# Optimization experiments

Measured on AMD Instinct MI355X. Metric: run time of the kernel, lower is better.

## Reference

```python
import jax, jax.numpy as jnp
import numpy as np

IN_F = 4096
OUT_F = 11008
GROUP = 128
NGROUPS = IN_F // GROUP
MAX_INT = 15  # 2**4 - 1


def setup_inputs() -> dict:
    key = jax.random.key(0)
    k1, k2, k3, k4, k5 = jax.random.split(key, 5)
    x = jax.random.normal(k1, (4, 2048, IN_F), dtype=jnp.float32)
    qweight = jax.random.randint(k2, (OUT_F, IN_F), 0, MAX_INT + 1, dtype=jnp.int32)
    scales = jax.random.uniform(k3, (OUT_F, NGROUPS), dtype=jnp.float32) * 0.01 + 1e-4
    zeros = jax.random.uniform(k4, (OUT_F, NGROUPS), dtype=jnp.float32) * MAX_INT
    b = jax.random.normal(k5, (OUT_F,), dtype=jnp.float32)
    return {"x": x, "qweight": qweight, "scales": scales, "zeros": zeros, "b": b}


def reference(x, qweight, scales, zeros, b):
    # Group-wise dequantization: W[o, i] = (q[o, i] - zeros[o, g(i)]) * scales[o, g(i)]
    s_rep = jnp.repeat(scales, GROUP, axis=1)  # [OUT_F, IN_F]
    z_rep = jnp.repeat(zeros, GROUP, axis=1)   # [OUT_F, IN_F]
    w_fp = (qweight.astype(x.dtype) - z_rep.astype(x.dtype)) * s_rep.astype(x.dtype)
    # F.linear: x @ W.T + b
    out = jnp.einsum('bsi,oi->bso', x, w_fp) + b.astype(x.dtype)
    return out
```

## Files before the change

kernel.cpp:

```cpp
#include <hip/hip_runtime.h>
#include <hip/hip_bf16.h>


#define K_DIM 4096
#define N_DIM 11008
#define M_DIM 8192
#define NGRP 32

typedef __bf16 bf16x8 __attribute__((ext_vector_type(8)));
typedef float f32x4 __attribute__((ext_vector_type(4)));
typedef unsigned short u16x8 __attribute__((ext_vector_type(8)));

__device__ __forceinline__ unsigned short f2bf(float f) {
  unsigned u = __builtin_bit_cast(unsigned, f);
  return (unsigned short)((u + 0x7FFFu + ((u >> 16) & 1u)) >> 16);
}

__device__ __forceinline__ void gload_lds16(const void* g, void* l) {
  __builtin_amdgcn_global_load_lds(
      (const __attribute__((address_space(1))) unsigned int*)(unsigned long long)g,
      (__attribute__((address_space(3))) unsigned int*)(unsigned int)(unsigned long long)l,
      16, 0, 0);
}

__global__ __launch_bounds__(256) void cvt_x_kernel(const float4* __restrict__ x4,
                                                    u16x8* __restrict__ xb) {
  int i = blockIdx.x * 256 + threadIdx.x;
  float4 a = x4[2 * i], b = x4[2 * i + 1];
  u16x8 r;
  r[0] = f2bf(a.x); r[1] = f2bf(a.y); r[2] = f2bf(a.z); r[3] = f2bf(a.w);
  r[4] = f2bf(b.x); r[5] = f2bf(b.y); r[6] = f2bf(b.z); r[7] = f2bf(b.w);
  xb[i] = r;
}

__global__ __launch_bounds__(256) void dequant_kernel(const int4* __restrict__ q4,
                                                      const float* __restrict__ scales,
                                                      const float* __restrict__ zeros,
                                                      u16x8* __restrict__ wb) {
  int t = blockIdx.x * 256 + threadIdx.x;
  int o = t >> 9;
  int j8 = t & 511;
  int g = j8 >> 4;
  float s = scales[o * NGRP + g];
  float z = zeros[o * NGRP + g];
  float nzs = -z * s;
  int4 qa = q4[2 * t], qb = q4[2 * t + 1];
  u16x8 r;
  r[0] = f2bf(fmaf((float)qa.x, s, nzs));
  r[1] = f2bf(fmaf((float)qa.y, s, nzs));
  r[2] = f2bf(fmaf((float)qa.z, s, nzs));
  r[3] = f2bf(fmaf((float)qa.w, s, nzs));
  r[4] = f2bf(fmaf((float)qb.x, s, nzs));
  r[5] = f2bf(fmaf((float)qb.y, s, nzs));
  r[6] = f2bf(fmaf((float)qb.z, s, nzs));
  r[7] = f2bf(fmaf((float)qb.w, s, nzs));
  wb[t] = r;
}


#define BAR() __builtin_amdgcn_s_barrier()
#define SCHED0() __builtin_amdgcn_sched_barrier(0)

__global__ __launch_bounds__(512, 2) void gemm_kernel(const unsigned short* __restrict__ A,
                                                      const unsigned short* __restrict__ B,
                                                      const float* __restrict__ bias,
                                                      float* __restrict__ C) {
  extern __shared__ unsigned short smem[];
  unsigned short* sAb = smem;
  unsigned short* sBb = smem + 32768;

  const int bid = blockIdx.x;
  const int swz = (bid & 7) * 172 + (bid >> 3);
  const int tm = swz / 43, tn = swz % 43;

  const int tid = threadIdx.x;
  const int w = tid >> 6, l = tid & 63;
  const int wr = w >> 2, wc = w & 3;

  const int dsto = w * 512 + l * 8;
  const int gs = (l & 7) ^ (l >> 3);
  const unsigned short* gA = A + (size_t)(tm * 256 + (tid >> 3)) * K_DIM + gs * 8;
  const unsigned short* gB = B + (size_t)(tn * 256 + (tid >> 3)) * K_DIM + gs * 8;

#define STG_A(tt, h, dst)                                                       \
  do {                                                                          \
    const unsigned short* _s = gA + (size_t)(h) * 128 * K_DIM + (tt) * 64;      \
    gload_lds16(_s, (dst) + dsto);                                              \
    gload_lds16(_s + 64 * K_DIM, (dst) + 4096 + dsto);                          \
  } while (0)
#define STG_B(tt, h, dst)                                                       \
  do {                                                                          \
    const unsigned short* _s = gB + (size_t)(h) * 128 * K_DIM + (tt) * 64;      \
    gload_lds16(_s, (dst) + dsto);                                              \
    gload_lds16(_s + 64 * K_DIM, (dst) + 4096 + dsto);                          \
  } while (0)

  const int fr = l & 15, sb = l >> 4, x7 = l & 7;
  const int abase = (wr * 64 + fr) * 64;
  const int bbase = (wc * 32 + fr) * 64;
  const int k0 = (sb ^ x7) * 8;
  const int k1 = ((sb + 4) ^ x7) * 8;

  bf16x8 av[4][2], bva[2][2], bvb[2][2];
  f32x4 acc[8][4] = {};

#define READ_A(half)                                                     \
  {                                                                      \
    _Pragma("unroll") for (int m = 0; m < 4; ++m) {                      \
      av[m][0] = *(const bf16x8*)((half) + abase + m * 1024 + k0);       \
      av[m][1] = *(const bf16x8*)((half) + abase + m * 1024 + k1);       \
    }                                                                    \
  }
#define READ_B(half, arr)                                                \
  {                                                                      \
    _Pragma("unroll") for (int n = 0; n < 2; ++n) {                      \
      arr[n][0] = *(const bf16x8*)((half) + bbase + n * 1024 + k0);      \
      arr[n][1] = *(const bf16x8*)((half) + bbase + n * 1024 + k1);      \
    }                                                                    \
  }
#define MFMA_Q(mh, nh, arr)                                                        \
  {                                                                                \
    __builtin_amdgcn_s_setprio(1);                                                 \
    _Pragma("unroll") for (int kk = 0; kk < 2; ++kk)                               \
    _Pragma("unroll") for (int m = 0; m < 4; ++m)                                  \
    _Pragma("unroll") for (int nn = 0; nn < 2; ++nn)                               \
      acc[(mh)*4 + m][(nh)*2 + nn] = __builtin_amdgcn_mfma_f32_16x16x32_bf16(      \
          av[m][kk], arr[nn][kk], acc[(mh)*4 + m][(nh)*2 + nn], 0, 0, 0);          \
    __builtin_amdgcn_s_setprio(0);                                                 \
  }

  STG_A(0, 0, sAb);
  STG_A(0, 1, sAb + 8192);
  STG_B(0, 0, sBb);
  STG_B(0, 1, sBb + 8192);
  STG_A(1, 0, sAb + 16384);
  STG_B(1, 1, sBb + 16384 + 8192);
  asm volatile("s_waitcnt vmcnt(4)" ::: "memory");
  BAR();
  SCHED0();

#pragma unroll 2
  for (int t = 0; t < 64; ++t) {
    const int p = t & 1;
    unsigned short* cA = sAb + p * 16384;
    unsigned short* cB = sBb + p * 16384;
    unsigned short* nA = sAb + (p ^ 1) * 16384;
    unsigned short* nB = sBb + (p ^ 1) * 16384;

    READ_A(cA);
    READ_B(cB, bva);
    if (t < 63) STG_A(t + 1, 1, nA + 8192);
    BAR();
    SCHED0();
    MFMA_Q(0, 0, bva);

    READ_B(cB + 8192, bvb);
    if (t < 63) STG_B(t + 1, 0, nB);
    BAR();
    SCHED0();
    MFMA_Q(0, 1, bvb);

    READ_A(cA + 8192);
    if (t < 62) STG_A(t + 2, 0, cA);
    BAR();
    SCHED0();
    MFMA_Q(1, 1, bvb);

    if (t < 62) STG_B(t + 2, 1, cB + 8192);
    MFMA_Q(1, 0, bva);
    if (t < 62) {
      asm volatile("s_waitcnt vmcnt(4)" ::: "memory");
    } else {
      asm volatile("s_waitcnt vmcnt(0)" ::: "memory");
    }
    BAR();
    SCHED0();
  }

  const int r0 = tm * 256 + wr * 64 + sb * 4;
  const int c0 = tn * 256 + wc * 32 + fr;
#pragma unroll
  for (int n = 0; n < 4; ++n) {
    const int col = c0 + (n >> 1) * 128 + (n & 1) * 16;
    const float bv = bias[col];
#pragma unroll
    for (int mi = 0; mi < 8; ++mi) {
      const int row = r0 + (mi >> 2) * 128 + (mi & 3) * 16;
#pragma unroll
      for (int jj = 0; jj < 4; ++jj)
        C[(size_t)(row + jj) * N_DIM + col] = acc[mi][n][jj] + bv;
    }
  }
}

extern "C" void kernel_launch(void* const* d_in, const int* in_sizes, int n_in,
                              void* d_out, int out_size, void* d_ws, size_t ws_size,
                              hipStream_t stream) {
  const float* x = (const float*)d_in[0];
  const int* qw = (const int*)d_in[1];
  const float* sc = (const float*)d_in[2];
  const float* zr = (const float*)d_in[3];
  const float* bs = (const float*)d_in[4];
  float* out = (float*)d_out;

  const size_t xb_bytes = (size_t)M_DIM * K_DIM * 2;
  const size_t wb_bytes = (size_t)N_DIM * K_DIM * 2;
  if (ws_size < xb_bytes + wb_bytes) return;

  unsigned short* xb = (unsigned short*)d_ws;
  unsigned short* wb = (unsigned short*)((char*)d_ws + xb_bytes);

  (void)hipFuncSetAttribute((const void*)gemm_kernel,
                            hipFuncAttributeMaxDynamicSharedMemorySize, 131072);

  cvt_x_kernel<<<(M_DIM * K_DIM / 8) / 256, 256, 0, stream>>>((const float4*)x, (u16x8*)xb);
  dequant_kernel<<<(N_DIM * K_DIM / 8) / 256, 256, 0, stream>>>((const int4*)qw, sc, zr,
                                                                (u16x8*)wb);
  gemm_kernel<<<(M_DIM / 256) * (N_DIM / 256), 512, 131072, stream>>>(xb, wb, bs, out);
}
```

Before: 733.9 us.

## Load B operand directly from global into registers, halve LDS usage

```diff
diff --git a/kernel.cpp b/kernel.cpp
--- a/kernel.cpp
+++ b/kernel.cpp
@@ -66,8 +66,8 @@
                                                       const float* __restrict__ bias,
                                                       float* __restrict__ C) {
   extern __shared__ unsigned short smem[];
-  unsigned short* sAb = smem;
-  unsigned short* sBb = smem + 32768;
+  unsigned short* s0 = smem;
+  unsigned short* s1 = smem + 16384;
 
   const int bid = blockIdx.x;
   const int swz = (bid & 7) * 172 + (bid >> 3);
@@ -80,7 +80,6 @@
   const int dsto = w * 512 + l * 8;
   const int gs = (l & 7) ^ (l >> 3);
   const unsigned short* gA = A + (size_t)(tm * 256 + (tid >> 3)) * K_DIM + gs * 8;
-  const unsigned short* gB = B + (size_t)(tn * 256 + (tid >> 3)) * K_DIM + gs * 8;
 
 #define STG_A(tt, h, dst)                                                       \
   do {                                                                          \
@@ -88,20 +87,16 @@
     gload_lds16(_s, (dst) + dsto);                                              \
     gload_lds16(_s + 64 * K_DIM, (dst) + 4096 + dsto);                          \
   } while (0)
-#define STG_B(tt, h, dst)                                                       \
-  do {                                                                          \
-    const unsigned short* _s = gB + (size_t)(h) * 128 * K_DIM + (tt) * 64;      \
-    gload_lds16(_s, (dst) + dsto);                                              \
-    gload_lds16(_s + 64 * K_DIM, (dst) + 4096 + dsto);                          \
-  } while (0)
 
   const int fr = l & 15, sb = l >> 4, x7 = l & 7;
   const int abase = (wr * 64 + fr) * 64;
-  const int bbase = (wc * 32 + fr) * 64;
   const int k0 = (sb ^ x7) * 8;
   const int k1 = ((sb + 4) ^ x7) * 8;
 
-  bf16x8 av[4][2], bva[2][2], bvb[2][2];
+  const unsigned short* gBbase = B + (size_t)(tn * 256 + wc * 32 + fr) * K_DIM + sb * 8;
+
+  bf16x8 av[4][2];
+  bf16x8 bE[2][2][2], bO[2][2][2];
   f32x4 acc[8][4] = {};
 
 #define READ_A(half)                                                     \
@@ -111,70 +106,73 @@
       av[m][1] = *(const bf16x8*)((half) + abase + m * 1024 + k1);       \
     }                                                                    \
   }
-#define READ_B(half, arr)                                                \
-  {                                                                      \
-    _Pragma("unroll") for (int n = 0; n < 2; ++n) {                      \
-      arr[n][0] = *(const bf16x8*)((half) + bbase + n * 1024 + k0);      \
-      arr[n][1] = *(const bf16x8*)((half) + bbase + n * 1024 + k1);      \
-    }                                                                    \
-  }
-#define MFMA_Q(mh, nh, arr)                                                        \
+#define LOAD_B(dst, kp)                                                            \
+  {                                                                                \
+    _Pragma("unroll") for (int h = 0; h < 2; ++h)                                  \
+    _Pragma("unroll") for (int nn = 0; nn < 2; ++nn)                               \
+    _Pragma("unroll") for (int kk = 0; kk < 2; ++kk)                               \
+      dst[h][nn][kk] = *(const bf16x8*)((kp) + (size_t)h * (128 * K_DIM) +         \
+                                        nn * (16 * K_DIM) + kk * 32);              \
+  }
+#define MFMA_Q(mh, h, B2)                                                          \
   {                                                                                \
     __builtin_amdgcn_s_setprio(1);                                                 \
     _Pragma("unroll") for (int kk = 0; kk < 2; ++kk)                               \
     _Pragma("unroll") for (int m = 0; m < 4; ++m)                                  \
     _Pragma("unroll") for (int nn = 0; nn < 2; ++nn)                               \
-      acc[(mh)*4 + m][(nh)*2 + nn] = __builtin_amdgcn_mfma_f32_16x16x32_bf16(      \
-          av[m][kk], arr[nn][kk], acc[(mh)*4 + m][(nh)*2 + nn], 0, 0, 0);          \
+      acc[(mh)*4 + m][(h)*2 + nn] = __builtin_amdgcn_mfma_f32_16x16x32_bf16(       \
+          av[m][kk], B2[nn][kk], acc[(mh)*4 + m][(h)*2 + nn], 0, 0, 0);            \
     __builtin_amdgcn_s_setprio(0);                                                 \
   }
 
-  STG_A(0, 0, sAb);
-  STG_A(0, 1, sAb + 8192);
-  STG_B(0, 0, sBb);
-  STG_B(0, 1, sBb + 8192);
-  STG_A(1, 0, sAb + 16384);
-  STG_B(1, 1, sBb + 16384 + 8192);
-  asm volatile("s_waitcnt vmcnt(4)" ::: "memory");
+  STG_A(0, 0, s0);
+  STG_A(0, 1, s0 + 8192);
+  SCHED0();
+  LOAD_B(bE, gBbase);
+  asm volatile("s_waitcnt vmcnt(8)" ::: "memory");
   BAR();
   SCHED0();
 
-#pragma unroll 2
-  for (int t = 0; t < 64; ++t) {
-    const int p = t & 1;
-    unsigned short* cA = sAb + p * 16384;
-    unsigned short* cB = sBb + p * 16384;
-    unsigned short* nA = sAb + (p ^ 1) * 16384;
-    unsigned short* nB = sBb + (p ^ 1) * 16384;
-
-    READ_A(cA);
-    READ_B(cB, bva);
-    if (t < 63) STG_A(t + 1, 1, nA + 8192);
+  const unsigned short* kp = gBbase;
+  for (int tt = 0; tt < 32; ++tt) {
+    const int t1 = 2 * tt + 1;
+
+    READ_A(s0);
+    STG_A(t1, 0, s1);
+    STG_A(t1, 1, s1 + 8192);
+    SCHED0();
+    MFMA_Q(0, 0, bE[0]);
+    MFMA_Q(0, 1, bE[1]);
+    SCHED0();
+    LOAD_B(bO, kp + 64);
+    SCHED0();
+    READ_A(s0 + 8192);
+    MFMA_Q(1, 1, bE[1]);
+    MFMA_Q(1, 0, bE[0]);
+    asm volatile("s_waitcnt vmcnt(8)" ::: "memory");
     BAR();
     SCHED0();
-    MFMA_Q(0, 0, bva);
-
-    READ_B(cB + 8192, bvb);
-    if (t < 63) STG_B(t + 1, 0, nB);
-    BAR();
-    SCHED0();
-    MFMA_Q(0, 1, bvb);
-
-    READ_A(cA + 8192);
-    if (t < 62) STG_A(t + 2, 0, cA);
-    BAR();
-    SCHED0();
-    MFMA_Q(1, 1, bvb);
-
-    if (t < 62) STG_B(t + 2, 1, cB + 8192);
-    MFMA_Q(1, 0, bva);
-    if (t < 62) {
-      asm volatile("s_waitcnt vmcnt(4)" ::: "memory");
-    } else {
-      asm volatile("s_waitcnt vmcnt(0)" ::: "memory");
+
+    READ_A(s1);
+    if (tt < 31) {
+      STG_A(t1 + 1, 0, s0);
+      STG_A(t1 + 1, 1, s0 + 8192);
     }
-    BAR();
-    SCHED0();
+    SCHED0();
+    MFMA_Q(0, 0, bO[0]);
+    MFMA_Q(0, 1, bO[1]);
+    SCHED0();
+    if (tt < 31) LOAD_B(bE, kp + 128);
+    SCHED0();
+    READ_A(s1 + 8192);
+    MFMA_Q(1, 1, bO[1]);
+    MFMA_Q(1, 0, bO[0]);
+    if (tt < 31) {
+      asm volatile("s_waitcnt vmcnt(8)" ::: "memory");
+      BAR();
+      SCHED0();
+    }
+    kp += 128;
   }
 
   const int r0 = tm * 256 + wr * 64 + sb * 4;
@@ -211,10 +209,10 @@
   unsigned short* wb = (unsigned short*)((char*)d_ws + xb_bytes);
 
   (void)hipFuncSetAttribute((const void*)gemm_kernel,
-                            hipFuncAttributeMaxDynamicSharedMemorySize, 131072);
+                            hipFuncAttributeMaxDynamicSharedMemorySize, 65536);
 
   cvt_x_kernel<<<(M_DIM * K_DIM / 8) / 256, 256, 0, stream>>>((const float4*)x, (u16x8*)xb);
   dequant_kernel<<<(N_DIM * K_DIM / 8) / 256, 256, 0, stream>>>((const int4*)qw, sc, zr,
                                                                 (u16x8*)wb);
-  gemm_kernel<<<(M_DIM / 256) * (N_DIM / 256), 512, 131072, stream>>>(xb, wb, bs, out);
-}
+  gemm_kernel<<<(M_DIM / 256) * (N_DIM / 256), 512, 65536, stream>>>(xb, wb, bs, out);
+}
```

After: 1.048 ms. +42.8%, slower.

## Replace staggered half-tile prefetch with simple full-tile double buffering

Applied to the files above, without the earlier changes.

```diff
diff --git a/kernel.cpp b/kernel.cpp
--- a/kernel.cpp
+++ b/kernel.cpp
@@ -57,7 +57,6 @@
   wb[t] = r;
 }
 
-
 #define BAR() __builtin_amdgcn_s_barrier()
 #define SCHED0() __builtin_amdgcn_sched_barrier(0)
 
@@ -129,52 +128,38 @@
     __builtin_amdgcn_s_setprio(0);                                                 \
   }
 
+#define TILE(tnext, curA, curB, nxtA, nxtB, has_next)                    \
+  {                                                                      \
+    if (has_next) {                                                      \
+      STG_A(tnext, 0, nxtA);                                             \
+      STG_A(tnext, 1, (nxtA) + 8192);                                    \
+      STG_B(tnext, 0, nxtB);                                             \
+      STG_B(tnext, 1, (nxtB) + 8192);                                    \
+    }                                                                    \
+    READ_A(curA);                                                        \
+    READ_B(curB, bva);                                                   \
+    READ_B((curB) + 8192, bvb);                                          \
+    MFMA_Q(0, 0, bva);                                                   \
+    MFMA_Q(0, 1, bvb);                                                   \
+    READ_A((curA) + 8192);                                               \
+    MFMA_Q(1, 1, bvb);                                                   \
+    MFMA_Q(1, 0, bva);                                                   \
+    asm volatile("s_waitcnt vmcnt(0)" ::: "memory");                     \
+    BAR();                                                               \
+    SCHED0();                                                            \
+  }
+
   STG_A(0, 0, sAb);
   STG_A(0, 1, sAb + 8192);
   STG_B(0, 0, sBb);
   STG_B(0, 1, sBb + 8192);
-  STG_A(1, 0, sAb + 16384);
-  STG_B(1, 1, sBb + 16384 + 8192);
-  asm volatile("s_waitcnt vmcnt(4)" ::: "memory");
+  asm volatile("s_waitcnt vmcnt(0)" ::: "memory");
   BAR();
   SCHED0();
 
-#pragma unroll 2
-  for (int t = 0; t < 64; ++t) {
-    const int p = t & 1;
-    unsigned short* cA = sAb + p * 16384;
-    unsigned short* cB = sBb + p * 16384;
-    unsigned short* nA = sAb + (p ^ 1) * 16384;
-    unsigned short* nB = sBb + (p ^ 1) * 16384;
-
-    READ_A(cA);
-    READ_B(cB, bva);
-    if (t < 63) STG_A(t + 1, 1, nA + 8192);
-    BAR();
-    SCHED0();
-    MFMA_Q(0, 0, bva);
-
-    READ_B(cB + 8192, bvb);
-    if (t < 63) STG_B(t + 1, 0, nB);
-    BAR();
-    SCHED0();
-    MFMA_Q(0, 1, bvb);
-
-    READ_A(cA + 8192);
-    if (t < 62) STG_A(t + 2, 0, cA);
-    BAR();
-    SCHED0();
-    MFMA_Q(1, 1, bvb);
-
-    if (t < 62) STG_B(t + 2, 1, cB + 8192);
-    MFMA_Q(1, 0, bva);
-    if (t < 62) {
-      asm volatile("s_waitcnt vmcnt(4)" ::: "memory");
-    } else {
-      asm volatile("s_waitcnt vmcnt(0)" ::: "memory");
-    }
-    BAR();
-    SCHED0();
+  for (int tt = 0; tt < 32; ++tt) {
+    TILE(2 * tt + 1, sAb, sBb, sAb + 16384, sBb + 16384, 1);
+    TILE(2 * tt + 2, sAb + 16384, sBb + 16384, sAb, sBb, (tt < 31));
   }
 
   const int r0 = tm * 256 + wr * 64 + sb * 4;
```

After: 751.6 us. 1.02x slower.
